# Kernel tuning notes

Measured on AMD Instinct MI355X. Metric: run time of the kernel, lower is better.

The kernel has to match this reference:

```python
import jax, jax.numpy as jnp
import numpy as np

_PADDING_NUM = -1


def setup_inputs() -> dict:
    key = jax.random.key(0)
    B, M, S, C = 4096, 64, 64, 4096  # batch, num_buckets, multiplex_count, channels
    x = jax.random.normal(key, (B, C), dtype=jnp.float32)
    # Full packing: each slot holds a unique object index (no padding).
    assignments = jnp.arange(B, dtype=jnp.int32).reshape(M, S)
    return {"x": x, "assignments": assignments}


def reference(x, assignments):
    """Mux (dispatch) then demux (combine) via precomputed one-hot transition matrices.

    x:           (B, C)  data-space tensor
    assignments: (M, S)  object index per (bucket, slot); _PADDING_NUM (-1) -> zero slot
    returns demuxed (B, C): data-space tensor recovered from multiplex space.
    """
    B = x.shape[0]
    valid = (assignments >= 0)  # (M, S)
    # Transition matrix: (M, S, B); padding slots map to all-zero rows.
    T = jax.nn.one_hot(jnp.where(valid, assignments, 0), B, dtype=x.dtype)
    T = T * valid[..., None].astype(x.dtype)
    # mux: place each valid object into its (bucket, slot); padding slots are zeros.
    muxed = jnp.einsum('msb,bc->msc', T, x)  # (M, S, C)
    # demux: gather slots back to data space in object-index order.
    demuxed = jnp.einsum('msb,msc->bc', T, muxed)  # (B, C)
    return demuxed
```

## Files before the change

### kernel.cpp

```cpp
#include <hip/hip_runtime.h>


#define BLOCK 256
#define C_VEC 1024
#define VPT 4
#define MS_VEC 1024
#define APT 4

__global__ __launch_bounds__(BLOCK) void mux_fused_kernel(
    const float4* __restrict__ x,
    const int4* __restrict__ a4,
    float4* __restrict__ out) {
    const int b = blockIdx.x;
    const int tid = threadIdx.x;

    const long base = (long)b * C_VEC;
    float4 v[VPT];
#pragma unroll
    for (int k = 0; k < VPT; ++k)
        v[k] = x[base + tid + BLOCK * k];

    int local = 0;
#pragma unroll
    for (int k = 0; k < APT; ++k) {
        int4 a = a4[tid + BLOCK * k];
        local += (a.x == b) + (a.y == b) + (a.z == b) + (a.w == b);
    }

#pragma unroll
    for (int off = 32; off > 0; off >>= 1)
        local += __shfl_down(local, off, 64);

    __shared__ int wave_sum[BLOCK / 64];
    __shared__ float s_scale;
    const int wave = tid >> 6;
    if ((tid & 63) == 0) wave_sum[wave] = local;
    __syncthreads();
    if (tid == 0)
        s_scale = (float)(wave_sum[0] + wave_sum[1] + wave_sum[2] + wave_sum[3]);
    __syncthreads();
    const float s = s_scale;

#pragma unroll
    for (int k = 0; k < VPT; ++k) {
        float4 w = v[k];
        w.x *= s; w.y *= s; w.z *= s; w.w *= s;
        out[base + tid + BLOCK * k] = w;
    }
}

extern "C" void kernel_launch(void* const* d_in, const int* in_sizes, int n_in,
                              void* d_out, int out_size, void* d_ws, size_t ws_size,
                              hipStream_t stream) {
    const float* x = (const float*)d_in[0];
    const int* assignments = (const int*)d_in[1];
    float* out = (float*)d_out;

    const int B = 4096;
    mux_fused_kernel<<<dim3(B), dim3(BLOCK), 0, stream>>>(
        (const float4*)x, (const int4*)assignments, (float4*)out);
}
```

Baseline: 112.1 us.

## Process four rows per block with packed count reduction

```diff
diff --git a/kernel.cpp b/kernel.cpp
--- a/kernel.cpp
+++ b/kernel.cpp
@@ -2,50 +2,64 @@
 
 
 #define BLOCK 256
+#define R 4
 #define C_VEC 1024
-#define VPT 4
-#define MS_VEC 1024
+#define KPT 4
 #define APT 4
 
+typedef float v4f __attribute__((ext_vector_type(4)));
+
 __global__ __launch_bounds__(BLOCK) void mux_fused_kernel(
-    const float4* __restrict__ x,
+    const v4f* __restrict__ x,
     const int4* __restrict__ a4,
-    float4* __restrict__ out) {
-    const int b = blockIdx.x;
+    v4f* __restrict__ out) {
     const int tid = threadIdx.x;
+    const int r0 = blockIdx.x * R;
 
-    const long base = (long)b * C_VEC;
-    float4 v[VPT];
-#pragma unroll
-    for (int k = 0; k < VPT; ++k)
-        v[k] = x[base + tid + BLOCK * k];
-
-    int local = 0;
+    int p01 = 0, p23 = 0;
 #pragma unroll
     for (int k = 0; k < APT; ++k) {
         int4 a = a4[tid + BLOCK * k];
-        local += (a.x == b) + (a.y == b) + (a.z == b) + (a.w == b);
+#pragma unroll
+        for (int c = 0; c < 4; ++c) {
+            int av = (c == 0) ? a.x : (c == 1) ? a.y : (c == 2) ? a.z : a.w;
+            int d = av - r0;
+            p01 += (d == 0) + ((d == 1) << 16);
+            p23 += (d == 2) + ((d == 3) << 16);
+        }
     }
 
 #pragma unroll
-    for (int off = 32; off > 0; off >>= 1)
-        local += __shfl_down(local, off, 64);
+    for (int off = 32; off > 0; off >>= 1) {
+        p01 += __shfl_xor(p01, off, 64);
+        p23 += __shfl_xor(p23, off, 64);
+    }
 
-    __shared__ int wave_sum[BLOCK / 64];
-    __shared__ float s_scale;
+    __shared__ int2 wsum[BLOCK / 64];
     const int wave = tid >> 6;
-    if ((tid & 63) == 0) wave_sum[wave] = local;
+    if ((tid & 63) == 0) wsum[wave] = make_int2(p01, p23);
     __syncthreads();
-    if (tid == 0)
-        s_scale = (float)(wave_sum[0] + wave_sum[1] + wave_sum[2] + wave_sum[3]);
-    __syncthreads();
-    const float s = s_scale;
+    int t01 = 0, t23 = 0;
+#pragma unroll
+    for (int w = 0; w < BLOCK / 64; ++w) { t01 += wsum[w].x; t23 += wsum[w].y; }
+
+    float s[R];
+    s[0] = (float)(t01 & 0xFFFF);
+    s[1] = (float)(t01 >> 16);
+    s[2] = (float)(t23 & 0xFFFF);
+    s[3] = (float)(t23 >> 16);
 
 #pragma unroll
-    for (int k = 0; k < VPT; ++k) {
-        float4 w = v[k];
-        w.x *= s; w.y *= s; w.z *= s; w.w *= s;
-        out[base + tid + BLOCK * k] = w;
+    for (int j = 0; j < R; ++j) {
+        const long base = (long)(r0 + j) * C_VEC;
+        const float sj = s[j];
+#pragma unroll
+        for (int k = 0; k < KPT; ++k) {
+            const long i = base + tid + BLOCK * k;
+            v4f v = x[i];
+            v *= sj;
+            out[i] = v;
+        }
     }
 }
 
@@ -57,6 +71,6 @@
     float* out = (float*)d_out;
 
     const int B = 4096;
-    mux_fused_kernel<<<dim3(B), dim3(BLOCK), 0, stream>>>(
-        (const float4*)x, (const int4*)assignments, (float4*)out);
+    mux_fused_kernel<<<dim3(B / R), dim3(BLOCK), 0, stream>>>(
+        (const v4f*)x, (const int4*)assignments, (v4f*)out);
 }
```

Measured after the change: 113.3 us. Within noise of the previous version (+1.1%).
